# Kernel optimization log

Measured on AMD Instinct MI355X. Metric: run time of the kernel, lower is better.

Reference implementation:

```python
import jax, jax.numpy as jnp
import numpy as np


def hard_sigmoid(x):
    # Keras hard_sigmoid: clip(0.2*x + 0.5, 0, 1)
    return jnp.clip(x * 0.2 + 0.5, 0.0, 1.0)


def conv2d_same(x, w):
    # x: [B,H,W,Cin], w: [kh,kw,Cin,Cout]
    return jax.lax.conv_general_dilated(
        x, w, window_strides=(1, 1), padding='SAME',
        dimension_numbers=('NHWC', 'HWIO', 'NHWC'))


def convlstm2d(x, Wx, Wh, b):
    # x: [B,T,H,W,Cin]; Wx: [k,k,Cin,4*Cout]; Wh: [k,k,Cout,4*Cout]; b: [4*Cout]
    B, T, H, W, _ = x.shape
    Cout = Wh.shape[2]
    h0 = jnp.zeros((B, H, W, Cout), x.dtype)
    c0 = jnp.zeros((B, H, W, Cout), x.dtype)

    def step(carry, xt):
        h, c = carry
        z = conv2d_same(xt, Wx) + conv2d_same(h, Wh) + b
        i, f, g, o = jnp.split(z, 4, axis=-1)  # Keras gate order i,f,c,o
        c = hard_sigmoid(f) * c + hard_sigmoid(i) * jnp.tanh(g)
        h = hard_sigmoid(o) * jnp.tanh(c)
        return (h, c), h

    _, hs = jax.lax.scan(step, (h0, c0), jnp.moveaxis(x, 1, 0))
    return jnp.moveaxis(hs, 0, 1)  # [B,T,H,W,Cout]


def bn_inference(x, gamma, beta, mean, var, eps=1e-3):
    # Keras BatchNormalization default eps=1e-3, inference mode (training=False)
    return (x - mean) * jax.lax.rsqrt(var + eps) * gamma + beta


def upsample_2x2(x):
    # UpSampling3D(size=(1,2,2)) on [B,T,H,W,C]
    return jnp.repeat(jnp.repeat(x, 2, axis=2), 2, axis=3)


def deconv_block(x, Wx, Wh, b, g, be, mm, mv):
    return upsample_2x2(bn_inference(convlstm2d(x, Wx, Wh, b), g, be, mm, mv))


def setup_inputs() -> dict:
    key = jax.random.key(0)
    ks = jax.random.split(key, 32)
    B, T, H, W = 2, 8, 16, 16
    Cin = 192
    chans = [128, 64, 32]
    K = 3
    d = {'x': jax.random.normal(ks[0], (B, T, H, W, Cin), jnp.float32)}
    ci = Cin
    ki = 1
    for l, co in enumerate(chans, start=1):
        d[f'Wx{l}'] = jax.random.normal(ks[ki], (K, K, ci, 4 * co), jnp.float32) * 0.05; ki += 1
        d[f'Wh{l}'] = jax.random.normal(ks[ki], (K, K, co, 4 * co), jnp.float32) * 0.05; ki += 1
        d[f'b{l}'] = jnp.zeros((4 * co,), jnp.float32)
        d[f'g{l}'] = jax.random.uniform(ks[ki], (co,), jnp.float32) + 0.5; ki += 1
        d[f'be{l}'] = jax.random.normal(ks[ki], (co,), jnp.float32) * 0.1; ki += 1
        d[f'mm{l}'] = jax.random.normal(ks[ki], (co,), jnp.float32) * 0.1; ki += 1
        d[f'mv{l}'] = jax.random.uniform(ks[ki], (co,), jnp.float32) + 0.5; ki += 1
        ci = co
    return d


def reference(x, Wx1, Wh1, b1, g1, be1, mm1, mv1,
              Wx2, Wh2, b2, g2, be2, mm2, mv2,
              Wx3, Wh3, b3, g3, be3, mm3, mv3):
    x = deconv_block(x, Wx1, Wh1, b1, g1, be1, mm1, mv1)  # [2,8,32,32,128]
    x = deconv_block(x, Wx2, Wh2, b2, g2, be2, mm2, mv2)  # [2,8,64,64,64]
    x = deconv_block(x, Wx3, Wh3, b3, g3, be3, mm3, mv3)  # [2,8,128,128,32]
    return x
```

## Files before the change

### kernel.cpp

```cpp
#include <hip/hip_runtime.h>
#include <math.h>

#define BATCH 2
#define TSTEPS 8

typedef __attribute__((ext_vector_type(8))) short s16x8;
typedef __attribute__((ext_vector_type(4))) float f32x4;

__device__ __forceinline__ float hsig(float v){ return fminf(fmaxf(0.2f*v+0.5f,0.f),1.f); }
__device__ __forceinline__ ushort f2bf(float f){
    uint u = __builtin_bit_cast(uint, f);
    u = (u + 0x7FFFu + ((u >> 16) & 1u)) >> 16;
    return (ushort)u;
}
__device__ __forceinline__ uint pack2bf(float lo, float hi){
    return (uint)f2bf(lo) | ((uint)f2bf(hi) << 16);
}

template<int KCH, int KCHP, int Co>
__device__ __forceinline__ void packw(const float* __restrict__ W, ushort* __restrict__ dst, int d){
    int j = d & 7, lane = (d >> 3) & 63;
    int q = lane >> 4, l = lane & 15;
    int rest = d >> 9;
    int c = rest % KCHP, t_n = rest / KCHP;
    if (c >= KCH){ dst[d] = 0; return; }
    int k = c*32 + q*8 + j;
    int np = t_n*16 + l;
    int g = np & 3, co = np >> 2;
    dst[d] = f2bf(W[(size_t)k*(4*Co) + g*Co + co]);
}

#define SZ_X    786432
#define SZ_WX1  917504
#define SZ_WH1  589824
#define SZ_WX2  294912
#define SZ_WH2  163840
#define SZ_WX3   81920
#define SZ_WH3   49152
#define SZ_PREP (SZ_X+SZ_WX1+SZ_WH1+SZ_WX2+SZ_WH2+SZ_WX3+SZ_WH3)

struct Params {
    const float *x, *Wx1, *Wh1, *b1, *g1, *be1, *mm1, *mv1;
    const float *Wx2, *Wh2, *b2, *g2, *be2, *mm2, *mv2;
    const float *Wx3, *Wh3, *b3, *g3, *be3, *mm3, *mv3;
    float *c1, *c2, *c3;
    char  *zbase;
    ushort *xpad, *x2pad, *x3pad, *h1A, *h1B, *h2A, *h2B, *h3A, *h3B;
    ushort *Wxp1, *Wxp2, *Wxp3, *Whp1, *Whp2, *Whp3;
    float *out;
};

__device__ __forceinline__ void prep_elem(int i, const Params& p){
    if (i < SZ_X){
        int c = i % 192; int r = i / 192;
        int xx = r % 16; r /= 16; int yy = r % 16; int bt = r / 16;
        p.xpad[((size_t)bt*18*18 + (yy+1)*18 + (xx+1))*192 + c] = f2bf(p.x[i]);
        return;
    } i -= SZ_X;
    if (i < SZ_WX1){ packw<54,56,128>(p.Wx1, p.Wxp1, i); return; } i -= SZ_WX1;
    if (i < SZ_WH1){ packw<36,36,128>(p.Wh1, p.Whp1, i); return; } i -= SZ_WH1;
    if (i < SZ_WX2){ packw<36,36, 64>(p.Wx2, p.Wxp2, i); return; } i -= SZ_WX2;
    if (i < SZ_WH2){ packw<18,20, 64>(p.Wh2, p.Whp2, i); return; } i -= SZ_WH2;
    if (i < SZ_WX3){ packw<18,20, 32>(p.Wx3, p.Wxp3, i); return; } i -= SZ_WX3;
    if (i < SZ_WH3){ packw< 9,12, 32>(p.Wh3, p.Whp3, i); }
}

__global__ __launch_bounds__(256) void prep_kernel_g(Params p){
    int i = blockIdx.x*256 + threadIdx.x;
    if (i < SZ_PREP) prep_elem(i, p);
}

template<int CI, int CO, int H, int W, int OUT_BF16, int NCPB>
__device__ __forceinline__ void fused_role(char* smem, int lbid, int t, int first,
    const ushort* __restrict__ Apad, const ushort* __restrict__ Wxpk,
    const ushort* __restrict__ hprev, const ushort* __restrict__ Whpk,
    const float* __restrict__ bias,
    ushort* __restrict__ hnew, float* __restrict__ cst,
    const float* __restrict__ gamma, const float* __restrict__ beta,
    const float* __restrict__ mmean, const float* __restrict__ mvar,
    void* __restrict__ outp)
{
    constexpr int W_T = (W < 32) ? W : 32;
    constexpr int PR = (32/W_T) + 2, PPX = W_T + 2;
    constexpr int PCI = CI + 8, PCO = CO + 8;
    constexpr int KX = 9*CI/32, CPTX = CI/32;
    constexpr int KH = 9*CO/32, CPTH = CO/32;
    constexpr int KXP = (KX + 3) & ~3, KHP = (KH + 3) & ~3;
    constexpr int NJX = KXP/4, NJH = KHP/4;
    constexpr int HW = H*W, HP = H+2, WP = W+2;
    constexpr int CH8X = CI/8, CH8H = CO/8;
    constexpr int TOTX = PR*PPX*CH8X, TOTH = PR*PPX*CH8H;
    constexpr int PT = (BATCH*HW)/32;

    ushort* patch = (ushort*)smem;
    float* Zs = (float*)smem;
    float* Hs = (float*)(smem + NCPB*18432);

    const int tid = threadIdx.x, lane = tid & 63, wave = tid >> 6;
    const int quad = lane >> 4, l16 = lane & 15;
    const int pxt = lbid % PT, colB = lbid / PT;
    const int m0 = pxt * 32;
    const int b2 = m0 / HW, rem = m0 - b2*HW;
    const int y0 = rem / W, x0 = rem - (rem/W)*W;
    const int bt = b2*TSTEPS + t;

    f32x4 acc[NCPB][2][2] = {};

    int labaseX[2], labaseH[2];
    #pragma unroll
    for (int s = 0; s < 2; ++s){
        int pp = s*16 + l16;
        int rp = pp / W_T, xp = pp - rp*W_T;
        labaseX[s] = (rp*PPX + xp)*PCI + quad*8;
        labaseH[s] = (rp*PPX + xp)*PCO + quad*8;
    }

    {
        const ushort* gsrc = Apad + (size_t)bt*HP*WP*CI;
        for (int c = tid; c < TOTX; c += 256){
            int pix = c / CH8X, ch = c - pix*CH8X;
            int prow = pix / PPX, ppx = pix - prow*PPX;
            *(uint4*)&patch[pix*PCI + ch*8] =
                *(const uint4*)(gsrc + ((size_t)(y0+prow)*WP + (x0+ppx))*CI + ch*8);
        }
        __syncthreads();

        const ushort* bp[NCPB][2];
        #pragma unroll
        for (int cc = 0; cc < NCPB; ++cc){
            const int tn = (colB*NCPB + cc)*2;
            bp[cc][0] = Wxpk + ((size_t)tn*KXP*64 + lane)*8;
            bp[cc][1] = Wxpk + ((size_t)(tn+1)*KXP*64 + lane)*8;
        }
        #pragma unroll
        for (int j = 0; j < NJX; ++j){
            const int it = wave + 4*j;
            const int itA = (it < KX) ? it : 0;
            const int tap = itA / CPTX, ci0 = (itA - tap*CPTX)*32;
            const int kh = tap/3, kw = tap - (tap/3)*3;
            const int off = (kh*PPX + kw)*PCI + ci0;
            s16x8 a0 = *(const s16x8*)&patch[labaseX[0] + off];
            s16x8 a1 = *(const s16x8*)&patch[labaseX[1] + off];
            #pragma unroll
            for (int cc = 0; cc < NCPB; ++cc){
                s16x8 b0 = *(const s16x8*)(bp[cc][0] + (size_t)it*512);
                s16x8 b1 = *(const s16x8*)(bp[cc][1] + (size_t)it*512);
                acc[cc][0][0] = __builtin_amdgcn_mfma_f32_16x16x32_bf16(a0, b0, acc[cc][0][0], 0,0,0);
                acc[cc][0][1] = __builtin_amdgcn_mfma_f32_16x16x32_bf16(a0, b1, acc[cc][0][1], 0,0,0);
                acc[cc][1][0] = __builtin_amdgcn_mfma_f32_16x16x32_bf16(a1, b0, acc[cc][1][0], 0,0,0);
                acc[cc][1][1] = __builtin_amdgcn_mfma_f32_16x16x32_bf16(a1, b1, acc[cc][1][1], 0,0,0);
            }
        }
        __syncthreads();
    }

    if (!first){
        const ushort* gsrc = hprev + (size_t)b2*HP*WP*CO;
        for (int c = tid; c < TOTH; c += 256){
            int pix = c / CH8H, ch = c - pix*CH8H;
            int prow = pix / PPX, ppx = pix - prow*PPX;
            *(uint4*)&patch[pix*PCO + ch*8] =
                *(const uint4*)(gsrc + ((size_t)(y0+prow)*WP + (x0+ppx))*CO + ch*8);
        }
        __syncthreads();

        const ushort* bp[NCPB][2];
        #pragma unroll
        for (int cc = 0; cc < NCPB; ++cc){
            const int tn = (colB*NCPB + cc)*2;
            bp[cc][0] = Whpk + ((size_t)tn*KHP*64 + lane)*8;
            bp[cc][1] = Whpk + ((size_t)(tn+1)*KHP*64 + lane)*8;
        }
        #pragma unroll
        for (int j = 0; j < NJH; ++j){
            const int it = wave + 4*j;
            const int itA = (it < KH) ? it : 0;
            const int tap = itA / CPTH, ci0 = (itA - tap*CPTH)*32;
            const int kh = tap/3, kw = tap - (tap/3)*3;
            const int off = (kh*PPX + kw)*PCO + ci0;
            s16x8 a0 = *(const s16x8*)&patch[labaseH[0] + off];
            s16x8 a1 = *(const s16x8*)&patch[labaseH[1] + off];
            #pragma unroll
            for (int cc = 0; cc < NCPB; ++cc){
                s16x8 b0 = *(const s16x8*)(bp[cc][0] + (size_t)it*512);
                s16x8 b1 = *(const s16x8*)(bp[cc][1] + (size_t)it*512);
                acc[cc][0][0] = __builtin_amdgcn_mfma_f32_16x16x32_bf16(a0, b0, acc[cc][0][0], 0,0,0);
                acc[cc][0][1] = __builtin_amdgcn_mfma_f32_16x16x32_bf16(a0, b1, acc[cc][0][1], 0,0,0);
                acc[cc][1][0] = __builtin_amdgcn_mfma_f32_16x16x32_bf16(a1, b0, acc[cc][1][0], 0,0,0);
                acc[cc][1][1] = __builtin_amdgcn_mfma_f32_16x16x32_bf16(a1, b1, acc[cc][1][1], 0,0,0);
            }
        }
        __syncthreads();
    }

    #pragma unroll
    for (int cc = 0; cc < NCPB; ++cc)
        #pragma unroll
        for (int s = 0; s < 2; ++s)
            #pragma unroll
            for (int nt = 0; nt < 2; ++nt)
                #pragma unroll
                for (int r = 0; r < 4; ++r)
                    Zs[cc*4608 + (wave*32 + s*16 + quad*4 + r)*36 + nt*16 + l16] = acc[cc][s][nt][r];
    __syncthreads();

    #pragma unroll
    for (int cc = 0; cc < NCPB; ++cc){
        const int px = tid >> 3, coin = tid & 7;
        const int m = m0 + px;
        const int rr = m - b2*HW;
        const int co = (colB*NCPB + cc)*8 + coin;
        float zi = 0.f, zf = 0.f, zg = 0.f, zo = 0.f;
        #pragma unroll
        for (int w = 0; w < 4; ++w){
            const float4 s = *(const float4*)&Zs[cc*4608 + (w*32 + px)*36 + coin*4];
            zi += s.x; zf += s.y; zg += s.z; zo += s.w;
        }
        zi += bias[0*CO + co]; zf += bias[1*CO + co];
        zg += bias[2*CO + co]; zo += bias[3*CO + co];
        const float iv = hsig(zi), fv = hsig(zf);
        const float gv = tanhf(zg), ov = hsig(zo);
        const float cold = first ? 0.f : cst[(size_t)m*CO + co];
        const float cn = fv*cold + iv*gv;
        cst[(size_t)m*CO + co] = cn;
        const float h = ov * tanhf(cn);
        const int y = rr / W, x = rr - (rr/W)*W;
        hnew[((size_t)b2*HP*WP + (y+1)*WP + (x+1))*CO + co] = f2bf(h);
        Hs[cc*256 + px*8 + coin] = (h - mmean[co])*rsqrtf(mvar[co]+1e-3f)*gamma[co] + beta[co];
    }
    __syncthreads();

    #pragma unroll
    for (int cc = 0; cc < NCPB; ++cc){
        const int co0 = (colB*NCPB + cc)*8;
        if (OUT_BF16){
            if (tid < 128){
                const int px = tid >> 2, q = tid & 3;
                const int ypos = q >> 1, xpos = q & 1;
                const int m = m0 + px;
                const int rr = m - b2*HW;
                const int y = rr / W, x = rr - (rr/W)*W;
                const float* hs = &Hs[cc*256 + px*8];
                uint4 v;
                v.x = pack2bf(hs[0], hs[1]); v.y = pack2bf(hs[2], hs[3]);
                v.z = pack2bf(hs[4], hs[5]); v.w = pack2bf(hs[6], hs[7]);
                ushort* o = (ushort*)outp;
                const size_t opix = ((size_t)bt*(2*H+2) + 2*y+1+ypos)*(size_t)(2*W+2) + 2*x+1+xpos;
                *(uint4*)&o[opix*CO + co0] = v;
            }
        } else {
            const int px = tid >> 3, q = (tid >> 1) & 3, half = tid & 1;
            const int ypos = q >> 1, xpos = q & 1;
            const int m = m0 + px;
            const int rr = m - b2*HW;
            const int y = rr / W, x = rr - (rr/W)*W;
            float4 v = *(const float4*)&Hs[cc*256 + px*8 + half*4];
            float* o = (float*)outp;
            const size_t opix = ((size_t)bt*(2*H) + 2*y+ypos)*(size_t)(2*W) + 2*x+xpos;
            *(float4*)&o[opix*CO + co0 + half*4] = v;
        }
    }
}

__global__ __launch_bounds__(256, 4) void mega(Params p, int e1, int e2,
                                               int t1, int t2, int t3)
{
    __shared__ __align__(16) char smem[38912];
    const int bid = blockIdx.x;
    if (bid < e1){
        const ushort* hp = (t1 & 1) ? p.h1B : p.h1A;
        ushort*       hn = (t1 & 1) ? p.h1A : p.h1B;
        fused_role<192,128,16,16,1,1>(smem, bid, t1, t1==0,
            p.xpad, p.Wxp1, hp, p.Whp1, p.b1, hn, p.c1,
            p.g1, p.be1, p.mm1, p.mv1, p.x2pad);
    } else if (bid < e2){
        const ushort* hp = (t2 & 1) ? p.h2B : p.h2A;
        ushort*       hn = (t2 & 1) ? p.h2A : p.h2B;
        fused_role<128,64,32,32,1,2>(smem, bid - e1, t2, t2==0,
            p.x2pad, p.Wxp2, hp, p.Whp2, p.b2, hn, p.c2,
            p.g2, p.be2, p.mm2, p.mv2, p.x3pad);
    } else {
        const ushort* hp = (t3 & 1) ? p.h3B : p.h3A;
        ushort*       hn = (t3 & 1) ? p.h3A : p.h3B;
        fused_role<64,32,64,64,0,2>(smem, bid - e2, t3, t3==0,
            p.x3pad, p.Wxp3, hp, p.Whp3, p.b3, hn, p.c3,
            p.g3, p.be3, p.mm3, p.mv3, p.out);
    }
}

extern "C" void kernel_launch(void* const* d_in, const int* in_sizes, int n_in,
                              void* d_out, int out_size, void* d_ws, size_t ws_size,
                              hipStream_t stream) {
    Params p;
    p.x   = (const float*)d_in[0];
    p.Wx1 = (const float*)d_in[1];  p.Wh1 = (const float*)d_in[2];
    p.b1  = (const float*)d_in[3];  p.g1  = (const float*)d_in[4];
    p.be1 = (const float*)d_in[5];  p.mm1 = (const float*)d_in[6];
    p.mv1 = (const float*)d_in[7];
    p.Wx2 = (const float*)d_in[8];  p.Wh2 = (const float*)d_in[9];
    p.b2  = (const float*)d_in[10]; p.g2  = (const float*)d_in[11];
    p.be2 = (const float*)d_in[12]; p.mm2 = (const float*)d_in[13];
    p.mv2 = (const float*)d_in[14];
    p.Wx3 = (const float*)d_in[15]; p.Wh3 = (const float*)d_in[16];
    p.b3  = (const float*)d_in[17]; p.g3  = (const float*)d_in[18];
    p.be3 = (const float*)d_in[19]; p.mm3 = (const float*)d_in[20];
    p.mv3 = (const float*)d_in[21];

    char* ws = (char*)d_ws;
    size_t off = 0;
    auto alloc = [&](size_t bytes) { char* q = ws + off; off += (bytes + 255) & ~(size_t)255; return q; };

    p.c1  = (float*)alloc(65536ull * 4);
    p.c2  = (float*)alloc(131072ull * 4);
    p.c3  = (float*)alloc(262144ull * 4);

    p.zbase = alloc(17685504ull);
    p.xpad  = (ushort*)p.zbase;
    p.x2pad = p.xpad  + 995328;
    p.x3pad = p.x2pad + 2367488;
    p.h1A   = p.x3pad + 4460544;
    p.h1B   = p.h1A + 82944;
    p.h2A   = p.h1B + 82944;
    p.h2B   = p.h2A + 147968;
    p.h3A   = p.h2B + 147968;
    p.h3B   = p.h3A + 278784;

    p.Wxp1 = (ushort*)alloc((size_t)SZ_WX1 * 2);
    p.Wxp2 = (ushort*)alloc((size_t)SZ_WX2 * 2);
    p.Wxp3 = (ushort*)alloc((size_t)SZ_WX3 * 2);
    p.Whp1 = (ushort*)alloc((size_t)SZ_WH1 * 2);
    p.Whp2 = (ushort*)alloc((size_t)SZ_WH2 * 2);
    p.Whp3 = (ushort*)alloc((size_t)SZ_WH3 * 2);

    p.out = (float*)d_out;

    hipMemsetAsync(p.zbase, 0, 17685504ull, stream);

    prep_kernel_g<<<(SZ_PREP + 255) / 256, 256, 0, stream>>>(p);

    for (int j = 0; j <= 9; ++j){
        const int aS1 = (j <= 7);
        const int aS2 = (j >= 1 && j <= 8);
        const int aS3 = (j >= 2);
        const int e1 = aS1 ? 256 : 0;
        const int e2 = e1 + (aS2 ? 256 : 0);
        const int e3 = e2 + (aS3 ? 512 : 0);
        const int t1 = aS1 ? j     : 0;
        const int t2 = aS2 ? j - 1 : 0;
        const int t3 = aS3 ? j - 2 : 0;
        mega<<<dim3(e3), 256, 0, stream>>>(p, e1, e2, t1, t2, t3);
    }
}
```

Before: 257.2 us.

## Fuse memset into prep kernel and prefetch hidden-state patch into registers

Removes the separate hipMemsetAsync and folds zeroing of the padded scratch buffers into the prep kernel. The input x is now written vectorized, eight bf16 values per thread including the zero halo, instead of one scalar per element. Inside the fused ConvLSTM role, the global loads of the previous hidden-state patch are issued into registers before the input-weight MFMA loop, so their latency overlaps compute. The cost is higher register pressure from the hpf prefetch buffer, and the hand-computed zero-tail offset must exactly cover the h buffers.

```diff
diff --git a/kernel.cpp b/kernel.cpp
--- a/kernel.cpp
+++ b/kernel.cpp
@@ -30,14 +30,17 @@
     dst[d] = f2bf(W[(size_t)k*(4*Co) + g*Co + co]);
 }
 
-#define SZ_X    786432
 #define SZ_WX1  917504
 #define SZ_WH1  589824
 #define SZ_WX2  294912
 #define SZ_WH2  163840
 #define SZ_WX3   81920
 #define SZ_WH3   49152
-#define SZ_PREP (SZ_X+SZ_WX1+SZ_WH1+SZ_WX2+SZ_WH2+SZ_WX3+SZ_WH3)
+#define SZ_W    (SZ_WX1+SZ_WH1+SZ_WX2+SZ_WH2+SZ_WX3+SZ_WH3)
+
+#define XP4     124416
+#define ZTAIL   980928
+#define TOT_PREP (XP4 + SZ_W + ZTAIL)
 
 struct Params {
     const float *x, *Wx1, *Wh1, *b1, *g1, *be1, *mm1, *mv1;
@@ -50,24 +53,32 @@
     float *out;
 };
 
-__device__ __forceinline__ void prep_elem(int i, const Params& p){
-    if (i < SZ_X){
-        int c = i % 192; int r = i / 192;
-        int xx = r % 16; r /= 16; int yy = r % 16; int bt = r / 16;
-        p.xpad[((size_t)bt*18*18 + (yy+1)*18 + (xx+1))*192 + c] = f2bf(p.x[i]);
+__global__ __launch_bounds__(256) void prep_zero_g(Params p){
+    int i = blockIdx.x*256 + threadIdx.x;
+    if (i < XP4){
+        int c8 = i % 24; int r = i / 24;
+        int xx = r % 18; r /= 18; int yy = r % 18; int bt = r / 18;
+        uint4 v = {0,0,0,0};
+        if (xx >= 1 && xx <= 16 && yy >= 1 && yy <= 16){
+            const float* src = p.x + ((size_t)(bt*256 + (yy-1)*16 + (xx-1))*192 + c8*8);
+            float4 f0 = *(const float4*)src;
+            float4 f1 = *(const float4*)(src + 4);
+            v.x = pack2bf(f0.x, f0.y); v.y = pack2bf(f0.z, f0.w);
+            v.z = pack2bf(f1.x, f1.y); v.w = pack2bf(f1.z, f1.w);
+        }
+        *(uint4*)&p.xpad[((size_t)(bt*324 + yy*18 + xx)*192 + c8*8)] = v;
         return;
-    } i -= SZ_X;
+    } i -= XP4;
     if (i < SZ_WX1){ packw<54,56,128>(p.Wx1, p.Wxp1, i); return; } i -= SZ_WX1;
     if (i < SZ_WH1){ packw<36,36,128>(p.Wh1, p.Whp1, i); return; } i -= SZ_WH1;
     if (i < SZ_WX2){ packw<36,36, 64>(p.Wx2, p.Wxp2, i); return; } i -= SZ_WX2;
     if (i < SZ_WH2){ packw<18,20, 64>(p.Wh2, p.Whp2, i); return; } i -= SZ_WH2;
     if (i < SZ_WX3){ packw<18,20, 32>(p.Wx3, p.Wxp3, i); return; } i -= SZ_WX3;
-    if (i < SZ_WH3){ packw< 9,12, 32>(p.Wh3, p.Whp3, i); }
-}
-
-__global__ __launch_bounds__(256) void prep_kernel_g(Params p){
-    int i = blockIdx.x*256 + threadIdx.x;
-    if (i < SZ_PREP) prep_elem(i, p);
+    if (i < SZ_WH3){ packw< 9,12, 32>(p.Wh3, p.Whp3, i); return; } i -= SZ_WH3;
+    if (i < ZTAIL){
+        uint4 z = {0,0,0,0};
+        *((uint4*)(p.zbase + 1990656ull) + i) = z;
+    }
 }
 
 template<int CI, int CO, int H, int W, int OUT_BF16, int NCPB>
@@ -91,6 +102,7 @@
     constexpr int CH8X = CI/8, CH8H = CO/8;
     constexpr int TOTX = PR*PPX*CH8X, TOTH = PR*PPX*CH8H;
     constexpr int PT = (BATCH*HW)/32;
+    constexpr int NPF = (TOTH + 255)/256;
 
     ushort* patch = (ushort*)smem;
     float* Zs = (float*)smem;
@@ -123,8 +135,23 @@
             *(uint4*)&patch[pix*PCI + ch*8] =
                 *(const uint4*)(gsrc + ((size_t)(y0+prow)*WP + (x0+ppx))*CI + ch*8);
         }
-        __syncthreads();
-
+    }
+    uint4 hpf[NPF];
+    if (!first){
+        const ushort* gh = hprev + (size_t)b2*HP*WP*CO;
+        #pragma unroll
+        for (int k2 = 0; k2 < NPF; ++k2){
+            int c = tid + 256*k2;
+            if (c < TOTH){
+                int pix = c / CH8H, ch = c - pix*CH8H;
+                int prow = pix / PPX, ppx = pix - prow*PPX;
+                hpf[k2] = *(const uint4*)(gh + ((size_t)(y0+prow)*WP + (x0+ppx))*CO + ch*8);
+            }
+        }
+    }
+    __syncthreads();
+
+    {
         const ushort* bp[NCPB][2];
         #pragma unroll
         for (int cc = 0; cc < NCPB; ++cc){
@@ -151,16 +178,17 @@
                 acc[cc][1][1] = __builtin_amdgcn_mfma_f32_16x16x32_bf16(a1, b1, acc[cc][1][1], 0,0,0);
             }
         }
-        __syncthreads();
-    }
+    }
+    __syncthreads();
 
     if (!first){
-        const ushort* gsrc = hprev + (size_t)b2*HP*WP*CO;
-        for (int c = tid; c < TOTH; c += 256){
-            int pix = c / CH8H, ch = c - pix*CH8H;
-            int prow = pix / PPX, ppx = pix - prow*PPX;
-            *(uint4*)&patch[pix*PCO + ch*8] =
-                *(const uint4*)(gsrc + ((size_t)(y0+prow)*WP + (x0+ppx))*CO + ch*8);
+        #pragma unroll
+        for (int k2 = 0; k2 < NPF; ++k2){
+            int c = tid + 256*k2;
+            if (c < TOTH){
+                int pix = c / CH8H, ch = c - pix*CH8H;
+                *(uint4*)&patch[pix*PCO + ch*8] = hpf[k2];
+            }
         }
         __syncthreads();
 
@@ -334,9 +362,7 @@
 
     p.out = (float*)d_out;
 
-    hipMemsetAsync(p.zbase, 0, 17685504ull, stream);
-
-    prep_kernel_g<<<(SZ_PREP + 255) / 256, 256, 0, stream>>>(p);
+    prep_zero_g<<<(TOT_PREP + 255) / 256, 256, 0, stream>>>(p);
 
     for (int j = 0; j <= 9; ++j){
         const int aS1 = (j <= 7);
```

After: 278.1 us. +8.1%, slower.
